# Performance work log

Measured on AMD Instinct MI355X. Metric: run time of the kernel, lower is better.

Reference implementation:

```python
import jax, jax.numpy as jnp
import numpy as np

N, E, F, C = 50000, 640000, 128, 128  # nodes, edges, in_feat, hidden_channels
NEG_SLOPE = 0.2  # PyG GATConv default negative_slope


def setup_inputs() -> dict:
    key = jax.random.key(0)
    ks = jax.random.split(key, 16)
    s_in = 1.0 / np.sqrt(F)
    s_hid = 1.0 / np.sqrt(C)
    inp = {
        'x': jax.random.normal(ks[0], (N, F), jnp.float32),
        'edge_index': jax.random.randint(ks[1], (2, E), 0, N),
        # layer 1: GATConv (lin_src, lin_dst, att_src, att_dst, bias) + skip Linear
        'W1s': jax.random.normal(ks[2], (F, C), jnp.float32) * s_in,
        'W1d': jax.random.normal(ks[3], (F, C), jnp.float32) * s_in,
        'a1s': jax.random.normal(ks[4], (C,), jnp.float32) * s_hid,
        'a1d': jax.random.normal(ks[5], (C,), jnp.float32) * s_hid,
        'b1': jnp.zeros((C,), jnp.float32),
        'Wl1': jax.random.normal(ks[6], (F, C), jnp.float32) * s_in,
        'bl1': jnp.zeros((C,), jnp.float32),
        # layer 2
        'W2s': jax.random.normal(ks[7], (C, C), jnp.float32) * s_hid,
        'W2d': jax.random.normal(ks[8], (C, C), jnp.float32) * s_hid,
        'a2s': jax.random.normal(ks[9], (C,), jnp.float32) * s_hid,
        'a2d': jax.random.normal(ks[10], (C,), jnp.float32) * s_hid,
        'b2': jnp.zeros((C,), jnp.float32),
        'Wl2': jax.random.normal(ks[11], (C, C), jnp.float32) * s_hid,
        'bl2': jnp.zeros((C,), jnp.float32),
    }
    return inp


def gat_conv(x, Ws, Wd, a_s, a_d, b, src, dst):
    # project once per node, not per edge
    h_src = x @ Ws                      # [N, C]
    h_dst = x @ Wd                      # [N, C]
    alpha_src = h_src @ a_s             # [N]
    alpha_dst = h_dst @ a_d             # [N]
    # attention logits on edges: LeakyReLU(a_src[j] + a_dst[i]) for edge j->i
    e = jax.nn.leaky_relu(alpha_src[src] + alpha_dst[dst], NEG_SLOPE)  # [E]
    # segment softmax over incoming edges of each destination node
    e_max = jax.ops.segment_max(e, dst, num_segments=N)                # [N]
    e_exp = jnp.exp(e - e_max[dst])                                    # [E]
    e_sum = jax.ops.segment_sum(e_exp, dst, num_segments=N)            # [N]
    alpha = e_exp / (e_sum[dst] + 1e-16)                               # [E]
    # weighted message gather + scatter-add aggregation
    out = jax.ops.segment_sum(h_src[src] * alpha[:, None], dst, num_segments=N)  # [N, C]
    return out + b


def reference(x, edge_index, W1s, W1d, a1s, a1d, b1, Wl1, bl1,
              W2s, W2d, a2s, a2d, b2, Wl2, bl2):
    src, dst = edge_index[0], edge_index[1]
    h = gat_conv(x, W1s, W1d, a1s, a1d, b1, src, dst) + x @ Wl1 + bl1
    h = jax.nn.relu(h)
    out = gat_conv(h, W2s, W2d, a2s, a2d, b2, src, dst) + h @ Wl2 + bl2
    return out
```

## Files before the change

kernel.cpp:

```cpp
#include <hip/hip_runtime.h>


#define NEG_SLOPE 0.2f
#define SCAN_T 256
#define SCAN_ELE 1024

typedef __attribute__((ext_vector_type(8))) short short8;
typedef __attribute__((ext_vector_type(4))) float f32x4;

__device__ __forceinline__ unsigned short f2bf(float f) {
  unsigned u = __float_as_uint(f);
  u += 0x7FFF + ((u >> 16) & 1);
  return (unsigned short)(u >> 16);
}

__global__ __launch_bounds__(256) void zero_kernel(int* __restrict__ p, int n) {
  int i = blockIdx.x * 256 + threadIdx.x;
  if (i < n) p[i] = 0;
}

__global__ __launch_bounds__(256) void count_kernel(const int* __restrict__ dst,
                                                    int* __restrict__ deg, int E) {
  int e = blockIdx.x * 256 + threadIdx.x;
  if (e < E) atomicAdd(&deg[dst[e]], 1);
}

__global__ __launch_bounds__(SCAN_T) void scan_pre(const int* __restrict__ deg,
                                                   int* __restrict__ bsum, int n) {
  __shared__ int red[SCAN_T];
  int b = blockIdx.x, t = threadIdx.x;
  int base = b * SCAN_ELE + t * 4;
  int s = 0;
#pragma unroll
  for (int j = 0; j < 4; ++j) {
    int i = base + j;
    if (i < n) s += deg[i];
  }
  red[t] = s;
  __syncthreads();
  for (int d = SCAN_T / 2; d > 0; d >>= 1) {
    if (t < d) red[t] += red[t + d];
    __syncthreads();
  }
  if (t == 0) bsum[b] = red[0];
}

__global__ __launch_bounds__(256) void scan_mid(const int* __restrict__ bsum,
                                                int* __restrict__ boff,
                                                int* __restrict__ off, int nb, int n) {
  __shared__ int sh[256];
  int t = threadIdx.x;
  int v = (t < nb) ? bsum[t] : 0;
  sh[t] = v;
  __syncthreads();
  for (int d = 1; d < 256; d <<= 1) {
    int u = (t >= d) ? sh[t - d] : 0;
    __syncthreads();
    sh[t] += u;
    __syncthreads();
  }
  if (t < nb) boff[t] = (t == 0) ? 0 : sh[t - 1];
  if (t == 255) off[n] = sh[255];
}

__global__ __launch_bounds__(SCAN_T) void scan_post(const int* __restrict__ deg,
                                                    const int* __restrict__ boff,
                                                    int* __restrict__ off,
                                                    int* __restrict__ cursor, int n) {
  __shared__ int tsum[SCAN_T];
  int b = blockIdx.x, t = threadIdx.x;
  int base = b * SCAN_ELE + t * 4;
  int v[4];
  int s = 0;
#pragma unroll
  for (int j = 0; j < 4; ++j) {
    int i = base + j;
    v[j] = (i < n) ? deg[i] : 0;
    s += v[j];
  }
  tsum[t] = s;
  __syncthreads();
  for (int d = 1; d < SCAN_T; d <<= 1) {
    int u = (t >= d) ? tsum[t - d] : 0;
    __syncthreads();
    tsum[t] += u;
    __syncthreads();
  }
  int run = boff[b] + ((t == 0) ? 0 : tsum[t - 1]);
#pragma unroll
  for (int j = 0; j < 4; ++j) {
    int i = base + j;
    if (i < n) {
      off[i] = run;
      cursor[i] = run;
      run += v[j];
    }
  }
}

__global__ __launch_bounds__(256) void scatter_kernel(const int* __restrict__ src,
                                                      const int* __restrict__ dst,
                                                      int* __restrict__ cursor,
                                                      int* __restrict__ ssorted, int E) {
  int e = blockIdx.x * 256 + threadIdx.x;
  if (e < E) {
    int d = dst[e];
    int pos = atomicAdd(&cursor[d], 1);
    ssorted[pos] = src[e];
  }
}

__global__ __launch_bounds__(512) void wv_kernel(
    const float* __restrict__ W1s, const float* __restrict__ a1s,
    const float* __restrict__ W1d, const float* __restrict__ a1d,
    const float* __restrict__ W2s, const float* __restrict__ a2s,
    const float* __restrict__ W2d, const float* __restrict__ a2d,
    float* __restrict__ wv) {
  int t = threadIdx.x;
  int which = t >> 7, f = t & 127;
  const float* W;
  const float* a;
  if (which == 0)      { W = W1s; a = a1s; }
  else if (which == 1) { W = W1d; a = a1d; }
  else if (which == 2) { W = W2s; a = a2s; }
  else                 { W = W2d; a = a2d; }
  float s = 0.f;
#pragma unroll 8
  for (int c = 0; c < 128; ++c) s += W[f * 128 + c] * a[c];
  wv[which * 128 + f] = s;
}

__global__ __launch_bounds__(256) void wtrans_all(const float* __restrict__ W1s,
                                                  const float* __restrict__ Wl1,
                                                  const float* __restrict__ W2s,
                                                  const float* __restrict__ Wl2,
                                                  unsigned short* __restrict__ Wt) {
  int idx = blockIdx.x * 256 + threadIdx.x;
  int which = idx >> 14;
  int j = idx & 16383;
  const float* W = (which == 0) ? W1s : (which == 1) ? Wl1 : (which == 2) ? W2s : Wl2;
  int k = j >> 7, c = j & 127;
  Wt[which * 16384 + c * 128 + k] = f2bf(W[k * 128 + c]);
}

__global__ __launch_bounds__(256) void prep1(const float* __restrict__ X,
                                             const float* __restrict__ wv,
                                             unsigned short* __restrict__ Xb,
                                             float* __restrict__ asrc,
                                             float* __restrict__ adst, int n) {
  int lane = threadIdx.x & 63;
  int wid = threadIdx.x >> 6;
  int node = blockIdx.x * 4 + wid;
  if (node >= n) return;
  float2 xv = ((const float2*)X)[(size_t)node * 64 + lane];
  float2 sv = ((const float2*)wv)[lane];
  float2 dv = ((const float2*)(wv + 128))[lane];
  unsigned pack = (unsigned)f2bf(xv.x) | ((unsigned)f2bf(xv.y) << 16);
  ((unsigned*)Xb)[(size_t)node * 64 + lane] = pack;
  float ds = xv.x * sv.x + xv.y * sv.y;
  float dd = xv.x * dv.x + xv.y * dv.y;
#pragma unroll
  for (int o = 32; o > 0; o >>= 1) {
    ds += __shfl_down(ds, o);
    dd += __shfl_down(dd, o);
  }
  if (lane == 0) {
    asrc[node] = ds;
    adst[node] = dd;
  }
}

#define SWZ(row, e) ((e) ^ (((row) & 7) << 3))

__global__ __launch_bounds__(256) void gemm_mfma(const unsigned short* __restrict__ Xb,
                                                 const unsigned short* __restrict__ WtA,
                                                 const unsigned short* __restrict__ WtB,
                                                 const float* __restrict__ biasb,
                                                 unsigned short* __restrict__ hsrc,
                                                 float* __restrict__ skip, int n) {
  __shared__ unsigned short sX[64 * 128];
  __shared__ unsigned short sW[128 * 128];
  int y = blockIdx.y;
  const unsigned short* Wt = (y == 0) ? WtA : WtB;
  int r0 = blockIdx.x * 64;
  int tid = threadIdx.x;

#pragma unroll
  for (int cch = 0; cch < 4; ++cch) {
    int id = tid + cch * 256;
    int r = id >> 4;
    int e = (id & 15) * 8;
    int gr = r0 + r;
    short8 v = (short8){0, 0, 0, 0, 0, 0, 0, 0};
    if (gr < n) v = *(const short8*)(Xb + (size_t)gr * 128 + e);
    *(short8*)&sX[r * 128 + SWZ(r, e)] = v;
  }
#pragma unroll
  for (int cch = 0; cch < 8; ++cch) {
    int id = tid + cch * 256;
    int r = id >> 4;
    int e = (id & 15) * 8;
    short8 v = *(const short8*)(Wt + r * 128 + e);
    *(short8*)&sW[r * 128 + SWZ(r, e)] = v;
  }
  __syncthreads();

  int w = tid >> 6, l = tid & 63;
  int q = l >> 4, fr = l & 15;
  int arow = w * 16 + fr;

  short8 af[4];
#pragma unroll
  for (int ks = 0; ks < 4; ++ks)
    af[ks] = *(short8*)&sX[arow * 128 + SWZ(arow, ks * 32 + q * 8)];

  f32x4 acc[8];
#pragma unroll
  for (int ct = 0; ct < 8; ++ct) acc[ct] = (f32x4){0.f, 0.f, 0.f, 0.f};

#pragma unroll
  for (int ct = 0; ct < 8; ++ct) {
    int brow = ct * 16 + fr;
#pragma unroll
    for (int ks = 0; ks < 4; ++ks) {
      short8 bf = *(short8*)&sW[brow * 128 + SWZ(brow, ks * 32 + q * 8)];
      acc[ct] = __builtin_amdgcn_mfma_f32_16x16x32_bf16(af[ks], bf, acc[ct], 0, 0, 0);
    }
  }

  if (y == 0) {
#pragma unroll
    for (int ct = 0; ct < 8; ++ct) {
#pragma unroll
      for (int i = 0; i < 4; ++i) {
        int grow = r0 + w * 16 + q * 4 + i;
        if (grow < n) hsrc[(size_t)grow * 128 + ct * 16 + fr] = f2bf(acc[ct][i]);
      }
    }
  } else {
#pragma unroll
    for (int ct = 0; ct < 8; ++ct) {
      float bv = biasb[ct * 16 + fr];
#pragma unroll
      for (int i = 0; i < 4; ++i) {
        int grow = r0 + w * 16 + q * 4 + i;
        if (grow < n) skip[(size_t)grow * 128 + ct * 16 + fr] = acc[ct][i] + bv;
      }
    }
  }
}

__global__ __launch_bounds__(256) void agg_fused(const int* __restrict__ off,
                                                 const int* __restrict__ ssorted,
                                                 const float* __restrict__ asrc,
                                                 const float* __restrict__ adst,
                                                 const unsigned short* __restrict__ hs,
                                                 const float* __restrict__ skip,
                                                 const float* __restrict__ bias,
                                                 float* __restrict__ outp,
                                                 unsigned short* __restrict__ xb,
                                                 const float* __restrict__ wv2,
                                                 float* __restrict__ asrc2,
                                                 float* __restrict__ adst2,
                                                 int relu, int n) {
  __shared__ float2 s_ae[4][64];
  int lane = threadIdx.x & 63;
  int wid = threadIdx.x >> 6;
  int i = blockIdx.x * 4 + wid;
  if (i >= n) return;
  int s0 = off[i], s1 = off[i + 1];
  float ad = adst[i];

  float mx = -1e30f;
  for (int s = s0 + lane; s < s1; s += 64) {
    float e = asrc[ssorted[s]] + ad;
    e = (e > 0.f) ? e : NEG_SLOPE * e;
    mx = fmaxf(mx, e);
  }
#pragma unroll
  for (int o = 32; o > 0; o >>= 1) mx = fmaxf(mx, __shfl_xor(mx, o));

  float accx0 = 0.f, accy0 = 0.f, accx1 = 0.f, accy1 = 0.f;
  float psum = 0.f;
  for (int cb = s0; cb < s1; cb += 64) {
    int m = min(64, s1 - cb);
    if (lane < m) {
      int sv = ssorted[cb + lane];
      float e = asrc[sv] + ad;
      e = (e > 0.f) ? e : NEG_SLOPE * e;
      float a = __expf(e - mx);
      psum += a;
      s_ae[wid][lane] = make_float2(a, __int_as_float(sv));
    }
    int j = 0;
    for (; j + 2 <= m; j += 2) {
      float2 p0 = s_ae[wid][j];
      float2 p1 = s_ae[wid][j + 1];
      unsigned v0 = *(const unsigned*)(hs + (size_t)__float_as_int(p0.y) * 128 + lane * 2);
      unsigned v1 = *(const unsigned*)(hs + (size_t)__float_as_int(p1.y) * 128 + lane * 2);
      accx0 += p0.x * __uint_as_float(v0 << 16);
      accy0 += p0.x * __uint_as_float(v0 & 0xFFFF0000u);
      accx1 += p1.x * __uint_as_float(v1 << 16);
      accy1 += p1.x * __uint_as_float(v1 & 0xFFFF0000u);
    }
    if (j < m) {
      float2 p0 = s_ae[wid][j];
      unsigned v0 = *(const unsigned*)(hs + (size_t)__float_as_int(p0.y) * 128 + lane * 2);
      accx0 += p0.x * __uint_as_float(v0 << 16);
      accy0 += p0.x * __uint_as_float(v0 & 0xFFFF0000u);
    }
  }
#pragma unroll
  for (int o = 32; o > 0; o >>= 1) psum += __shfl_xor(psum, o);
  float inv = 1.f / (psum + 1e-16f);

  float2 sk = ((const float2*)skip)[(size_t)i * 64 + lane];
  float2 bv = ((const float2*)bias)[lane];
  float vx = (accx0 + accx1) * inv + bv.x + sk.x;
  float vy = (accy0 + accy1) * inv + bv.y + sk.y;
  if (relu) { vx = fmaxf(vx, 0.f); vy = fmaxf(vy, 0.f); }
  if (outp) ((float2*)outp)[(size_t)i * 64 + lane] = make_float2(vx, vy);
  if (xb) {
    unsigned pack = (unsigned)f2bf(vx) | ((unsigned)f2bf(vy) << 16);
    ((unsigned*)xb)[(size_t)i * 64 + lane] = pack;
    float2 sv2 = ((const float2*)wv2)[lane];
    float2 dv2 = ((const float2*)(wv2 + 128))[lane];
    float ds = vx * sv2.x + vy * sv2.y;
    float dd = vx * dv2.x + vy * dv2.y;
#pragma unroll
    for (int o = 32; o > 0; o >>= 1) {
      ds += __shfl_down(ds, o);
      dd += __shfl_down(dd, o);
    }
    if (lane == 0) {
      asrc2[i] = ds;
      adst2[i] = dd;
    }
  }
}

extern "C" void kernel_launch(void* const* d_in, const int* in_sizes, int n_in,
                              void* d_out, int out_size, void* d_ws, size_t ws_size,
                              hipStream_t stream) {
  const float* x   = (const float*)d_in[0];
  const int*   ei  = (const int*)d_in[1];
  const float* W1s = (const float*)d_in[2];
  const float* W1d = (const float*)d_in[3];
  const float* a1s = (const float*)d_in[4];
  const float* a1d = (const float*)d_in[5];
  const float* b1  = (const float*)d_in[6];
  const float* Wl1 = (const float*)d_in[7];
  const float* bl1 = (const float*)d_in[8];
  const float* W2s = (const float*)d_in[9];
  const float* W2d = (const float*)d_in[10];
  const float* a2s = (const float*)d_in[11];
  const float* a2d = (const float*)d_in[12];
  const float* b2  = (const float*)d_in[13];
  const float* Wl2 = (const float*)d_in[14];
  const float* bl2 = (const float*)d_in[15];

  const int N = in_sizes[0] / 128;
  const int E = in_sizes[1] / 2;
  const int* srcp = ei;
  const int* dstp = ei + E;

  char* base = (char*)d_ws;
  size_t o = 0;
  auto alloc = [&](size_t bytes) -> void* {
    void* p = base + o;
    o += (bytes + 255) & ~(size_t)255;
    return p;
  };
  const int NB = (N + SCAN_ELE - 1) / SCAN_ELE;
  int*   deg     = (int*)alloc((size_t)N * 4);
  int*   off     = (int*)alloc((size_t)(N + 1) * 4);
  int*   cursor  = (int*)alloc((size_t)N * 4);
  int*   bsum    = (int*)alloc((size_t)NB * 4);
  int*   boff    = (int*)alloc((size_t)NB * 4);
  int*   ssorted = (int*)alloc((size_t)E * 4);
  float* asrcA   = (float*)alloc((size_t)N * 4);
  float* adstA   = (float*)alloc((size_t)N * 4);
  float* asrcB   = (float*)alloc((size_t)N * 4);
  float* adstB   = (float*)alloc((size_t)N * 4);
  float* wv      = (float*)alloc(4 * 128 * 4);
  unsigned short* Xb    = (unsigned short*)alloc((size_t)N * 128 * 2);
  unsigned short* Wt    = (unsigned short*)alloc(4 * 128 * 128 * 2);
  unsigned short* hsrcB = (unsigned short*)alloc((size_t)N * 128 * 2);
  float* skip    = (float*)alloc((size_t)N * 128 * 4);
  (void)ws_size; (void)n_in; (void)out_size;

  zero_kernel<<<(N + 255) / 256, 256, 0, stream>>>(deg, N);
  count_kernel<<<(E + 255) / 256, 256, 0, stream>>>(dstp, deg, E);
  scan_pre<<<NB, SCAN_T, 0, stream>>>(deg, bsum, N);
  scan_mid<<<1, 256, 0, stream>>>(bsum, boff, off, NB, N);
  scan_post<<<NB, SCAN_T, 0, stream>>>(deg, boff, off, cursor, N);
  scatter_kernel<<<(E + 255) / 256, 256, 0, stream>>>(srcp, dstp, cursor, ssorted, E);
  wv_kernel<<<1, 512, 0, stream>>>(W1s, a1s, W1d, a1d, W2s, a2s, W2d, a2d, wv);
  wtrans_all<<<256, 256, 0, stream>>>(W1s, Wl1, W2s, Wl2, Wt);

  dim3 ggrid((N + 63) / 64, 2);
  int nwb = (N + 3) / 4;

  prep1<<<nwb, 256, 0, stream>>>(x, wv, Xb, asrcA, adstA, N);
  gemm_mfma<<<ggrid, 256, 0, stream>>>(Xb, Wt, Wt + 16384, bl1, hsrcB, skip, N);
  agg_fused<<<nwb, 256, 0, stream>>>(off, ssorted, asrcA, adstA, hsrcB, skip, b1,
                                     nullptr, Xb, wv + 256, asrcB, adstB, 1, N);

  gemm_mfma<<<ggrid, 256, 0, stream>>>(Xb, Wt + 2 * 16384, Wt + 3 * 16384, bl2,
                                       hsrcB, skip, N);
  agg_fused<<<nwb, 256, 0, stream>>>(off, ssorted, asrcB, adstB, hsrcB, skip, b2,
                                     (float*)d_out, nullptr, nullptr, nullptr,
                                     nullptr, 0, N);
}
```

Measured before the change: 319.5 us.

## Drop softmax max pass, unroll gather by four, vectorize edge kernels, merge weight prep

Removes the per-node max-reduction pass in the attention aggregation and exponentiates the raw logits directly, saving one gather over the edges. The neighbor gather loop is unrolled to four independent accumulators for more memory-level parallelism. The count and scatter kernels now handle two edges per thread with int2 loads, and the attention-vector kernel is folded into the weight transpose kernel to save a launch. Skipping the max subtraction risks exp overflow for large logits.

```diff
diff --git a/kernel.cpp b/kernel.cpp
--- a/kernel.cpp
+++ b/kernel.cpp
@@ -13,6 +13,8 @@
   u += 0x7FFF + ((u >> 16) & 1);
   return (unsigned short)(u >> 16);
 }
+__device__ __forceinline__ float bflo(unsigned v) { return __uint_as_float(v << 16); }
+__device__ __forceinline__ float bfhi(unsigned v) { return __uint_as_float(v & 0xFFFF0000u); }
 
 __global__ __launch_bounds__(256) void zero_kernel(int* __restrict__ p, int n) {
   int i = blockIdx.x * 256 + threadIdx.x;
@@ -21,8 +23,14 @@
 
 __global__ __launch_bounds__(256) void count_kernel(const int* __restrict__ dst,
                                                     int* __restrict__ deg, int E) {
-  int e = blockIdx.x * 256 + threadIdx.x;
-  if (e < E) atomicAdd(&deg[dst[e]], 1);
+  int e = (blockIdx.x * 256 + threadIdx.x) * 2;
+  if (e + 1 < E) {
+    int2 d = *(const int2*)(dst + e);
+    atomicAdd(&deg[d.x], 1);
+    atomicAdd(&deg[d.y], 1);
+  } else if (e < E) {
+    atomicAdd(&deg[dst[e]], 1);
+  }
 }
 
 __global__ __launch_bounds__(SCAN_T) void scan_pre(const int* __restrict__ deg,
@@ -102,45 +110,51 @@
                                                       const int* __restrict__ dst,
                                                       int* __restrict__ cursor,
                                                       int* __restrict__ ssorted, int E) {
-  int e = blockIdx.x * 256 + threadIdx.x;
-  if (e < E) {
+  int e = (blockIdx.x * 256 + threadIdx.x) * 2;
+  if (e + 1 < E) {
+    int2 s = *(const int2*)(src + e);
+    int2 d = *(const int2*)(dst + e);
+    int p0 = atomicAdd(&cursor[d.x], 1);
+    ssorted[p0] = s.x;
+    int p1 = atomicAdd(&cursor[d.y], 1);
+    ssorted[p1] = s.y;
+  } else if (e < E) {
     int d = dst[e];
     int pos = atomicAdd(&cursor[d], 1);
     ssorted[pos] = src[e];
   }
 }
 
-__global__ __launch_bounds__(512) void wv_kernel(
-    const float* __restrict__ W1s, const float* __restrict__ a1s,
-    const float* __restrict__ W1d, const float* __restrict__ a1d,
-    const float* __restrict__ W2s, const float* __restrict__ a2s,
-    const float* __restrict__ W2d, const float* __restrict__ a2d,
-    float* __restrict__ wv) {
-  int t = threadIdx.x;
-  int which = t >> 7, f = t & 127;
-  const float* W;
-  const float* a;
-  if (which == 0)      { W = W1s; a = a1s; }
-  else if (which == 1) { W = W1d; a = a1d; }
-  else if (which == 2) { W = W2s; a = a2s; }
-  else                 { W = W2d; a = a2d; }
-  float s = 0.f;
+__global__ __launch_bounds__(256) void wtrans_all(
+    const float* __restrict__ W1s, const float* __restrict__ Wl1,
+    const float* __restrict__ W2s, const float* __restrict__ Wl2,
+    const float* __restrict__ a1s, const float* __restrict__ a1d,
+    const float* __restrict__ a2s, const float* __restrict__ a2d,
+    const float* __restrict__ W1d, const float* __restrict__ W2d,
+    unsigned short* __restrict__ Wt, float* __restrict__ wv) {
+  if (blockIdx.x < 256) {
+    int idx = blockIdx.x * 256 + threadIdx.x;
+    int which = idx >> 14;
+    int j = idx & 16383;
+    const float* W = (which == 0) ? W1s : (which == 1) ? Wl1 : (which == 2) ? W2s : Wl2;
+    int k = j >> 7, c = j & 127;
+    Wt[which * 16384 + c * 128 + k] = f2bf(W[k * 128 + c]);
+  } else {
+    for (int rep = 0; rep < 2; ++rep) {
+      int item = threadIdx.x + rep * 256;
+      int which = item >> 7, f = item & 127;
+      const float* W;
+      const float* a;
+      if (which == 0)      { W = W1s; a = a1s; }
+      else if (which == 1) { W = W1d; a = a1d; }
+      else if (which == 2) { W = W2s; a = a2s; }
+      else                 { W = W2d; a = a2d; }
+      float s = 0.f;
 #pragma unroll 8
-  for (int c = 0; c < 128; ++c) s += W[f * 128 + c] * a[c];
-  wv[which * 128 + f] = s;
-}
-
-__global__ __launch_bounds__(256) void wtrans_all(const float* __restrict__ W1s,
-                                                  const float* __restrict__ Wl1,
-                                                  const float* __restrict__ W2s,
-                                                  const float* __restrict__ Wl2,
-                                                  unsigned short* __restrict__ Wt) {
-  int idx = blockIdx.x * 256 + threadIdx.x;
-  int which = idx >> 14;
-  int j = idx & 16383;
-  const float* W = (which == 0) ? W1s : (which == 1) ? Wl1 : (which == 2) ? W2s : Wl2;
-  int k = j >> 7, c = j & 127;
-  Wt[which * 16384 + c * 128 + k] = f2bf(W[k * 128 + c]);
+      for (int c = 0; c < 128; ++c) s += W[f * 128 + c] * a[c];
+      wv[which * 128 + f] = s;
+    }
+  }
 }
 
 __global__ __launch_bounds__(256) void prep1(const float* __restrict__ X,
@@ -271,16 +285,8 @@
   int s0 = off[i], s1 = off[i + 1];
   float ad = adst[i];
 
-  float mx = -1e30f;
-  for (int s = s0 + lane; s < s1; s += 64) {
-    float e = asrc[ssorted[s]] + ad;
-    e = (e > 0.f) ? e : NEG_SLOPE * e;
-    mx = fmaxf(mx, e);
-  }
-#pragma unroll
-  for (int o = 32; o > 0; o >>= 1) mx = fmaxf(mx, __shfl_xor(mx, o));
-
-  float accx0 = 0.f, accy0 = 0.f, accx1 = 0.f, accy1 = 0.f;
+  float ax0 = 0.f, ay0 = 0.f, ax1 = 0.f, ay1 = 0.f;
+  float ax2 = 0.f, ay2 = 0.f, ax3 = 0.f, ay3 = 0.f;
   float psum = 0.f;
   for (int cb = s0; cb < s1; cb += 64) {
     int m = min(64, s1 - cb);
@@ -288,26 +294,29 @@
       int sv = ssorted[cb + lane];
       float e = asrc[sv] + ad;
       e = (e > 0.f) ? e : NEG_SLOPE * e;
-      float a = __expf(e - mx);
+      float a = __expf(e);
       psum += a;
       s_ae[wid][lane] = make_float2(a, __int_as_float(sv));
     }
     int j = 0;
-    for (; j + 2 <= m; j += 2) {
+    for (; j + 4 <= m; j += 4) {
       float2 p0 = s_ae[wid][j];
       float2 p1 = s_ae[wid][j + 1];
+      float2 p2 = s_ae[wid][j + 2];
+      float2 p3 = s_ae[wid][j + 3];
       unsigned v0 = *(const unsigned*)(hs + (size_t)__float_as_int(p0.y) * 128 + lane * 2);
       unsigned v1 = *(const unsigned*)(hs + (size_t)__float_as_int(p1.y) * 128 + lane * 2);
-      accx0 += p0.x * __uint_as_float(v0 << 16);
-      accy0 += p0.x * __uint_as_float(v0 & 0xFFFF0000u);
-      accx1 += p1.x * __uint_as_float(v1 << 16);
-      accy1 += p1.x * __uint_as_float(v1 & 0xFFFF0000u);
-    }
-    if (j < m) {
+      unsigned v2 = *(const unsigned*)(hs + (size_t)__float_as_int(p2.y) * 128 + lane * 2);
+      unsigned v3 = *(const unsigned*)(hs + (size_t)__float_as_int(p3.y) * 128 + lane * 2);
+      ax0 += p0.x * bflo(v0); ay0 += p0.x * bfhi(v0);
+      ax1 += p1.x * bflo(v1); ay1 += p1.x * bfhi(v1);
+      ax2 += p2.x * bflo(v2); ay2 += p2.x * bfhi(v2);
+      ax3 += p3.x * bflo(v3); ay3 += p3.x * bfhi(v3);
+    }
+    for (; j < m; ++j) {
       float2 p0 = s_ae[wid][j];
       unsigned v0 = *(const unsigned*)(hs + (size_t)__float_as_int(p0.y) * 128 + lane * 2);
-      accx0 += p0.x * __uint_as_float(v0 << 16);
-      accy0 += p0.x * __uint_as_float(v0 & 0xFFFF0000u);
+      ax0 += p0.x * bflo(v0); ay0 += p0.x * bfhi(v0);
     }
   }
 #pragma unroll
@@ -316,8 +325,8 @@
 
   float2 sk = ((const float2*)skip)[(size_t)i * 64 + lane];
   float2 bv = ((const float2*)bias)[lane];
-  float vx = (accx0 + accx1) * inv + bv.x + sk.x;
-  float vy = (accy0 + accy1) * inv + bv.y + sk.y;
+  float vx = ((ax0 + ax1) + (ax2 + ax3)) * inv + bv.x + sk.x;
+  float vy = ((ay0 + ay1) + (ay2 + ay3)) * inv + bv.y + sk.y;
   if (relu) { vx = fmaxf(vx, 0.f); vy = fmaxf(vy, 0.f); }
   if (outp) ((float2*)outp)[(size_t)i * 64 + lane] = make_float2(vx, vy);
   if (xb) {
@@ -390,13 +399,13 @@
   (void)ws_size; (void)n_in; (void)out_size;
 
   zero_kernel<<<(N + 255) / 256, 256, 0, stream>>>(deg, N);
-  count_kernel<<<(E + 255) / 256, 256, 0, stream>>>(dstp, deg, E);
+  count_kernel<<<(E / 2 + 255) / 256, 256, 0, stream>>>(dstp, deg, E);
   scan_pre<<<NB, SCAN_T, 0, stream>>>(deg, bsum, N);
   scan_mid<<<1, 256, 0, stream>>>(bsum, boff, off, NB, N);
   scan_post<<<NB, SCAN_T, 0, stream>>>(deg, boff, off, cursor, N);
-  scatter_kernel<<<(E + 255) / 256, 256, 0, stream>>>(srcp, dstp, cursor, ssorted, E);
-  wv_kernel<<<1, 512, 0, stream>>>(W1s, a1s, W1d, a1d, W2s, a2s, W2d, a2d, wv);
-  wtrans_all<<<256, 256, 0, stream>>>(W1s, Wl1, W2s, Wl2, Wt);
+  scatter_kernel<<<(E / 2 + 255) / 256, 256, 0, stream>>>(srcp, dstp, cursor, ssorted, E);
+  wtrans_all<<<257, 256, 0, stream>>>(W1s, Wl1, W2s, Wl2, a1s, a1d, a2s, a2d,
+                                      W1d, W2d, Wt, wv);
 
   dim3 ggrid((N + 63) / 64, 2);
   int nwb = (N + 3) / 4;
```

New measurement: 302.9 us. 5.2% less time.
